# Performance work log

Measured on AMD Instinct MI355X. Metric: run time of the kernel, lower is better.

Reference implementation:

```python
import jax, jax.numpy as jnp
import numpy as np

N_NODES = 100000
N_EDGES = 1600000
IN_DIM = 128
HID = 64
N_GRAPHS = 64
OUT_DIM = 2


def setup_inputs() -> dict:
    key = jax.random.key(0)
    ks = jax.random.split(key, 16)
    x = jax.random.normal(ks[0], (N_NODES, IN_DIM), dtype=jnp.float32)
    edge_index = jax.random.randint(ks[1], (2, N_EDGES), 0, N_NODES, dtype=jnp.int64)
    batch = jnp.sort(jax.random.randint(ks[2], (N_NODES,), 0, N_GRAPHS, dtype=jnp.int64))
    def glorot(k, fan_in, fan_out):
        s = jnp.sqrt(6.0 / (fan_in + fan_out)).astype(jnp.float32)
        return jax.random.uniform(k, (fan_in, fan_out), jnp.float32, -s, s)
    return {
        "x": x, "edge_index": edge_index, "batch": batch,
        "W1": glorot(ks[3], IN_DIM, HID), "b1": jnp.zeros((HID,), jnp.float32),
        "W2": glorot(ks[4], HID, HID),   "b2": jnp.zeros((HID,), jnp.float32),
        "W3": glorot(ks[5], HID, HID),   "b3": jnp.zeros((HID,), jnp.float32),
        "Wc1": glorot(ks[6], HID, HID // 2), "bc1": jnp.zeros((HID // 2,), jnp.float32),
        "Wc2": glorot(ks[7], HID // 2, OUT_DIM), "bc2": jnp.zeros((OUT_DIM,), jnp.float32),
    }


def reference(x, edge_index, batch, W1, b1, W2, b2, W3, b3, Wc1, bc1, Wc2, bc2):
    n = x.shape[0]
    # GCNConv: add self-loops, symmetric deg^{-1/2} normalization
    loop = jnp.arange(n, dtype=edge_index.dtype)
    src = jnp.concatenate([edge_index[0], loop])  # [E+N]
    dst = jnp.concatenate([edge_index[1], loop])
    deg = jax.ops.segment_sum(jnp.ones_like(dst, dtype=x.dtype), dst, num_segments=n)
    dis = jnp.where(deg > 0, jax.lax.rsqrt(deg), 0.0)  # deg^{-1/2}
    norm = (dis[src] * dis[dst])[:, None]  # [E+N, 1]

    def conv(h, W, b):
        h = h @ W                                   # [N, F_out]
        msg = h[src] * norm                         # edge-wise gather
        return jax.ops.segment_sum(msg, dst, num_segments=n) + b  # scatter-add

    h = jax.nn.relu(conv(x, W1, b1))     # dropout is identity at inference
    h = jax.nn.relu(conv(h, W2, b2))
    h = conv(h, W3, b3)

    # global_mean_pool over batch ids
    sums = jax.ops.segment_sum(h, batch, num_segments=N_GRAPHS)
    cnts = jax.ops.segment_sum(jnp.ones((n,), h.dtype), batch, num_segments=N_GRAPHS)
    pooled = sums / jnp.maximum(cnts, 1.0)[:, None]  # [G, HID]

    # classifier MLP
    hcls = jax.nn.relu(pooled @ Wc1 + bc1)
    return hcls @ Wc2 + bc2  # [G, OUT_DIM]
```

## Files before the change

kernel.cpp:

```cpp
#include <hip/hip_runtime.h>
#include <hip/hip_bf16.h>

#define N_NODES 100000
#define N_EDGES 1600000
#define IN_DIM 128
#define HID 64
#define N_GRAPHS 64
#define OUT_DIM 2

#define NB_BUCKETS ((N_NODES + 255) / 256)
#define CHUNK 4096
#define NCHUNKS ((N_EDGES + CHUNK - 1) / CHUNK)
#define ARENA_CAP 6144


__device__ inline unsigned f2bf_rne(float f) {
    unsigned u = __float_as_uint(f);
    u += 0x7FFFu + ((u >> 16) & 1u);
    return u >> 16;
}
__device__ inline unsigned pack2(float lo, float hi) {
    return f2bf_rne(lo) | (f2bf_rne(hi) << 16);
}
__device__ inline float bf_lo(unsigned w) { return __uint_as_float(w << 16); }
__device__ inline float bf_hi(unsigned w) { return __uint_as_float(w & 0xFFFF0000u); }
__device__ inline float2 bf_pair(unsigned w) {
    return make_float2(bf_lo(w), bf_hi(w));
}
__device__ inline void acc2(float2& a, float2 b) { a.x += b.x; a.y += b.y; }


__global__ void kb_scan(const int* __restrict__ bcount, int* __restrict__ bbase) {
    int lane = threadIdx.x;
    int carry = 0;
    for (int c = 0; c < (NB_BUCKETS + 63) / 64; ++c) {
        int idx = c * 64 + lane;
        int v = (idx < NB_BUCKETS) ? bcount[idx] : 0;
        int orig = v;
        for (int d = 1; d < 64; d <<= 1) {
            int u = __shfl_up(v, d);
            if (lane >= d) v += u;
        }
        if (idx < NB_BUCKETS) bbase[idx] = v - orig + carry;
        carry += __shfl(v, 63);
    }
    if (lane == 0) bbase[NB_BUCKETS] = carry;
}

__global__ __launch_bounds__(256) void kb_scatter(const int* __restrict__ src,
                                                  const int* __restrict__ dst,
                                                  int* __restrict__ bcount,
                                                  unsigned* __restrict__ arena) {
    __shared__ unsigned staged[CHUNK];
    __shared__ unsigned short sbuck[CHUNK];
    __shared__ int hist[NB_BUCKETS];
    __shared__ int lofs[NB_BUCKETS];
    __shared__ int lcur[NB_BUCKETS];
    __shared__ int gbase[NB_BUCKETS];
    int t = threadIdx.x;
    int lane = t & 63, wv = t >> 6;
    for (int i = t; i < NB_BUCKETS; i += 256) hist[i] = 0;
    __syncthreads();
    int chunk0 = blockIdx.x * CHUNK;
    int cN = min(CHUNK, N_EDGES - chunk0);
    for (int i = t; i < cN; i += 256) atomicAdd(&hist[dst[chunk0 + i] >> 8], 1);
    __syncthreads();
    if (wv == 0) {
        int carry = 0;
        for (int c = 0; c < (NB_BUCKETS + 63) / 64; ++c) {
            int idx = c * 64 + lane;
            int v = (idx < NB_BUCKETS) ? hist[idx] : 0;
            int orig = v;
            for (int d = 1; d < 64; d <<= 1) {
                int u = __shfl_up(v, d);
                if (lane >= d) v += u;
            }
            if (idx < NB_BUCKETS) lofs[idx] = v - orig + carry;
            carry += __shfl(v, 63);
        }
    }
    __syncthreads();
    for (int i = t; i < NB_BUCKETS; i += 256) {
        lcur[i] = lofs[i];
        gbase[i] = hist[i] ? (atomicAdd(&bcount[i], hist[i]) + i * ARENA_CAP) : 0;
    }
    __syncthreads();
    for (int i = t; i < cN; i += 256) {
        int e = chunk0 + i;
        int d = dst[e];
        int b = d >> 8;
        int lp = atomicAdd(&lcur[b], 1);
        staged[lp] = ((unsigned)src[e] << 8) | (unsigned)(d & 255);
        sbuck[lp] = (unsigned short)b;
    }
    __syncthreads();
    for (int p = t; p < cN; p += 256) {
        int b = sbuck[p];
        arena[gbase[b] + (p - lofs[b])] = staged[p];
    }
}

__global__ __launch_bounds__(256) void k_bfin(const unsigned* __restrict__ arena,
                                              const int* __restrict__ bbase,
                                              int* __restrict__ ssrc,
                                              int* __restrict__ off,
                                              float* __restrict__ dis) {
    __shared__ int cnt[256];
    __shared__ int lofs[256];
    __shared__ int lcur[256];
    int t = threadIdx.x;
    int lane = t & 63, wv = t >> 6;
    cnt[t] = 0;
    __syncthreads();
    int b = blockIdx.x;
    int lo = bbase[b];
    int cntB = bbase[b + 1] - lo;
    const unsigned* ap = arena + (size_t)b * ARENA_CAP;
    for (int e = t; e < cntB; e += 256) atomicAdd(&cnt[ap[e] & 255], 1);
    __syncthreads();
    if (wv == 0) {
        int carry = 0;
#pragma unroll
        for (int c = 0; c < 4; ++c) {
            int idx = c * 64 + lane;
            int v = cnt[idx];
            int orig = v;
            for (int d = 1; d < 64; d <<= 1) {
                int u = __shfl_up(v, d);
                if (lane >= d) v += u;
            }
            lofs[idx] = v - orig + carry;
            carry += __shfl(v, 63);
        }
    }
    __syncthreads();
    lcur[t] = lofs[t];
    int node = b * 256 + t;
    if (node < N_NODES) {
        off[node] = lo + lofs[t];
        dis[node] = rsqrtf((float)cnt[t] + 1.0f);
    }
    if (b == NB_BUCKETS - 1 && t == 0) off[N_NODES] = N_EDGES;
    __syncthreads();
    for (int e = t; e < cntB; e += 256) {
        unsigned pk = ap[e];
        int p = atomicAdd(&lcur[pk & 255u], 1);
        ssrc[lo + p] = (int)(pk >> 8);
    }
}


__global__ __launch_bounds__(256) void k_wprep(const float* __restrict__ W1,
                                               const float* __restrict__ W2,
                                               const float* __restrict__ W3,
                                               unsigned short* __restrict__ Wt1,
                                               unsigned short* __restrict__ Wt2,
                                               unsigned short* __restrict__ Wt3) {
    int t = blockIdx.x * 256 + threadIdx.x;
    if (t < 64 * 128) {
        int n = t >> 7, k = t & 127;
        Wt1[t] = (unsigned short)f2bf_rne(W1[k * 64 + n]);
    }
    if (t < 64 * 64) {
        int n = t >> 6, k = t & 63;
        Wt2[t] = (unsigned short)f2bf_rne(W2[k * 64 + n]);
        Wt3[t] = (unsigned short)f2bf_rne(W3[k * 64 + n]);
    }
}

template <int K, bool AF32>
__global__ __launch_bounds__(256) void k_gemm(const void* __restrict__ Ain,
                                              const unsigned short* __restrict__ Wt,
                                              const float* __restrict__ dis,
                                              unsigned* __restrict__ g16) {
    constexpr int PITCH = K + 8;
    constexpr int ABYTES = 2 * 64 * PITCH * 2;
    constexpr int CBYTES = 64 * 68 * 4;
    constexpr int SMEM = ABYTES > CBYTES ? ABYTES : CBYTES;
    __shared__ __align__(16) char smem[SMEM];
    short* As = (short*)smem;
    short* Bs = As + 64 * PITCH;
    float* Cs = (float*)smem;
    constexpr int CP = 68;

    int t = threadIdx.x, lane = t & 63, w = t >> 6;
    int row0 = blockIdx.x * 64;

    constexpr int UN = 64 * (K / 8);
#pragma unroll
    for (int u = t; u < UN; u += 256) {
        int r = u / (K / 8), c = u % (K / 8);
        int grow = row0 + r;
        grow = grow < N_NODES ? grow : N_NODES - 1;
        uint4 o;
        if (AF32) {
            const float* Ap = (const float*)Ain + (size_t)grow * K + c * 8;
            float4 f0 = *(const float4*)Ap;
            float4 f1 = *(const float4*)(Ap + 4);
            o.x = pack2(f0.x, f0.y); o.y = pack2(f0.z, f0.w);
            o.z = pack2(f1.x, f1.y); o.w = pack2(f1.z, f1.w);
        } else {
            o = ((const uint4*)Ain)[(size_t)grow * (K / 8) + c];
        }
        *(uint4*)&As[r * PITCH + c * 8] = o;
    }
#pragma unroll
    for (int u = t; u < UN; u += 256) {
        int n = u / (K / 8), c = u % (K / 8);
        *(uint4*)&Bs[n * PITCH + c * 8] = *(const uint4*)&Wt[n * K + c * 8];
    }
    __syncthreads();

    using frag = __attribute__((ext_vector_type(8))) short;
    using fragc = __attribute__((ext_vector_type(4))) float;
    fragc z = {0.f, 0.f, 0.f, 0.f};
    fragc acc[4] = {z, z, z, z};
    int m = lane & 15, quad = lane >> 4;
#pragma unroll
    for (int ks = 0; ks < K / 32; ++ks) {
        frag a = *(frag*)&As[(w * 16 + m) * PITCH + ks * 32 + quad * 8];
#pragma unroll
        for (int nt = 0; nt < 4; ++nt) {
            frag b = *(frag*)&Bs[(nt * 16 + m) * PITCH + ks * 32 + quad * 8];
            acc[nt] = __builtin_amdgcn_mfma_f32_16x16x32_bf16(a, b, acc[nt], 0, 0, 0);
        }
    }
    __syncthreads();
#pragma unroll
    for (int nt = 0; nt < 4; ++nt)
#pragma unroll
        for (int reg = 0; reg < 4; ++reg)
            Cs[(w * 16 + quad * 4 + reg) * CP + nt * 16 + m] = acc[nt][reg];
    __syncthreads();

    {
        int r = t >> 2, c0 = (t & 3) * 16;
        int grow = row0 + r;
        if (grow < N_NODES) {
            float dr = dis[grow];
            const float* cp = &Cs[r * CP + c0];
            uint4 o0, o1;
            o0.x = pack2(cp[0] * dr, cp[1] * dr);
            o0.y = pack2(cp[2] * dr, cp[3] * dr);
            o0.z = pack2(cp[4] * dr, cp[5] * dr);
            o0.w = pack2(cp[6] * dr, cp[7] * dr);
            o1.x = pack2(cp[8] * dr, cp[9] * dr);
            o1.y = pack2(cp[10] * dr, cp[11] * dr);
            o1.z = pack2(cp[12] * dr, cp[13] * dr);
            o1.w = pack2(cp[14] * dr, cp[15] * dr);
            ((uint4*)g16)[(size_t)grow * 8 + (c0 >> 3)] = o0;
            ((uint4*)g16)[(size_t)grow * 8 + (c0 >> 3) + 1] = o1;
        }
    }
}

template <bool RELU>
__global__ __launch_bounds__(256) void k_aggr(const unsigned* __restrict__ g16,
                                              const int* __restrict__ off,
                                              const int* __restrict__ ssrc,
                                              const float* __restrict__ dis,
                                              const float* __restrict__ bias,
                                              unsigned* __restrict__ h16) {
    int lane = threadIdx.x & 63, wv = threadIdx.x >> 6;
    int r8 = lane >> 3;
    int li = lane & 7;
    int row = blockIdx.x * 32 + wv * 8 + r8;
    if (row >= N_NODES) return;
    const uint4* g4 = (const uint4*)g16;
    float2 acc[4] = {make_float2(0.f, 0.f), make_float2(0.f, 0.f),
                     make_float2(0.f, 0.f), make_float2(0.f, 0.f)};
    int lo = off[row], hi = off[row + 1];
    int e = lo;
    for (; e + 1 < hi; e += 2) {
        unsigned o0 = (unsigned)ssrc[e] * 8u + (unsigned)li;
        unsigned o1 = (unsigned)ssrc[e + 1] * 8u + (unsigned)li;
        uint4 v0 = g4[o0];
        uint4 v1 = g4[o1];
        acc2(acc[0], bf_pair(v0.x)); acc2(acc[0], bf_pair(v1.x));
        acc2(acc[1], bf_pair(v0.y)); acc2(acc[1], bf_pair(v1.y));
        acc2(acc[2], bf_pair(v0.z)); acc2(acc[2], bf_pair(v1.z));
        acc2(acc[3], bf_pair(v0.w)); acc2(acc[3], bf_pair(v1.w));
    }
    if (e < hi) {
        unsigned o = (unsigned)ssrc[e] * 8u + (unsigned)li;
        uint4 v = g4[o];
        acc2(acc[0], bf_pair(v.x));
        acc2(acc[1], bf_pair(v.y));
        acc2(acc[2], bf_pair(v.z));
        acc2(acc[3], bf_pair(v.w));
    }
    unsigned base = (unsigned)row * 8u + (unsigned)li;
    uint4 sv = g4[base];
    float2 sp[4] = {bf_pair(sv.x), bf_pair(sv.y), bf_pair(sv.z), bf_pair(sv.w)};
    float dr = dis[row];
    float4 b0 = ((const float4*)bias)[li * 2];
    float4 b1 = ((const float4*)bias)[li * 2 + 1];
    float bb[8] = {b0.x, b0.y, b0.z, b0.w, b1.x, b1.y, b1.z, b1.w};
    float o[8];
#pragma unroll
    for (int j = 0; j < 4; ++j) {
        o[2 * j]     = dr * (acc[j].x + sp[j].x) + bb[2 * j];
        o[2 * j + 1] = dr * (acc[j].y + sp[j].y) + bb[2 * j + 1];
    }
    if (RELU) {
#pragma unroll
        for (int j = 0; j < 8; ++j) o[j] = fmaxf(o[j], 0.f);
    }
    uint4 wvo;
    wvo.x = pack2(o[0], o[1]);
    wvo.y = pack2(o[2], o[3]);
    wvo.z = pack2(o[4], o[5]);
    wvo.w = pack2(o[6], o[7]);
    ((uint4*)h16)[base] = wvo;
}


__global__ __launch_bounds__(256) void k_pool1(const unsigned short* __restrict__ h16,
                                               const int* __restrict__ batch,
                                               float* __restrict__ sums) {
    int lane = threadIdx.x & 63, wv = threadIdx.x >> 6;
    int node0 = blockIdx.x * 256 + wv * 64;
    int node1 = min(node0 + 64, N_NODES);
    float acc = 0.f;
    int cur = -1;
    for (int i = node0; i < node1; ++i) {
        int bi = batch[i];
        if (bi != cur) {
            if (cur >= 0) atomicAdd(&sums[cur * HID + lane], acc);
            acc = 0.f;
            cur = bi;
        }
        unsigned u = h16[(size_t)i * HID + lane];
        acc += __uint_as_float(u << 16);
    }
    if (cur >= 0) atomicAdd(&sums[cur * HID + lane], acc);
}

__device__ inline int lower_bound_batch(const int* batch, int key) {
    int lo = 0, hi = N_NODES;
    while (lo < hi) {
        int mid = (lo + hi) >> 1;
        if (batch[mid] < key) lo = mid + 1;
        else hi = mid;
    }
    return lo;
}

__global__ __launch_bounds__(256) void k_cls(const float* __restrict__ sums,
                                             const int* __restrict__ batch,
                                             const float* __restrict__ Wc1,
                                             const float* __restrict__ bc1,
                                             const float* __restrict__ Wc2,
                                             const float* __restrict__ bc2,
                                             float* __restrict__ out) {
    __shared__ float pooled[N_GRAPHS][HID];
    __shared__ float hc[N_GRAPHS][HID / 2];
    __shared__ float cnts[N_GRAPHS];
    int t = threadIdx.x;
    if (t < N_GRAPHS) {
        int lo = lower_bound_batch(batch, t);
        int hi = lower_bound_batch(batch, t + 1);
        cnts[t] = fmaxf((float)(hi - lo), 1.0f);
    }
    __syncthreads();
    for (int idx = t; idx < N_GRAPHS * HID; idx += 256) {
        int gi = idx >> 6;
        pooled[gi][idx & 63] = sums[idx] / cnts[gi];
    }
    __syncthreads();
    for (int idx = t; idx < N_GRAPHS * (HID / 2); idx += 256) {
        int gi = idx >> 5, f = idx & 31;
        float a = bc1[f];
#pragma unroll
        for (int k = 0; k < HID; ++k) a = fmaf(pooled[gi][k], Wc1[k * (HID / 2) + f], a);
        hc[gi][f] = fmaxf(a, 0.f);
    }
    __syncthreads();
    for (int idx = t; idx < N_GRAPHS * OUT_DIM; idx += 256) {
        int gi = idx >> 1, f = idx & 1;
        float a = bc2[f];
#pragma unroll
        for (int k = 0; k < HID / 2; ++k) a = fmaf(hc[gi][k], Wc2[k * OUT_DIM + f], a);
        out[gi * OUT_DIM + f] = a;
    }
}


extern "C" void kernel_launch(void* const* d_in, const int* in_sizes, int n_in,
                              void* d_out, int out_size, void* d_ws, size_t ws_size,
                              hipStream_t stream) {
    const float* x    = (const float*)d_in[0];
    const int*   eidx = (const int*)d_in[1];
    const int*   batch= (const int*)d_in[2];
    const float* W1 = (const float*)d_in[3];  const float* b1 = (const float*)d_in[4];
    const float* W2 = (const float*)d_in[5];  const float* b2 = (const float*)d_in[6];
    const float* W3 = (const float*)d_in[7];  const float* b3 = (const float*)d_in[8];
    const float* Wc1 = (const float*)d_in[9];  const float* bc1 = (const float*)d_in[10];
    const float* Wc2 = (const float*)d_in[11]; const float* bc2 = (const float*)d_in[12];
    float* out = (float*)d_out;

    const int* esrc = eidx;
    const int* edst = eidx + N_EDGES;

    size_t o = 0;
    auto alloc = [&](size_t bytes) {
        void* p = (char*)d_ws + o;
        o += (bytes + 255) & ~(size_t)255;
        return p;
    };
    int*            bcount = (int*)alloc((size_t)NB_BUCKETS * 4);
    int*            bbase  = (int*)alloc((size_t)(NB_BUCKETS + 1) * 4);
    float*          dis    = (float*)alloc((size_t)N_NODES * 4);
    unsigned*       arena  = (unsigned*)alloc((size_t)NB_BUCKETS * ARENA_CAP * 4);
    int*            ssrc   = (int*)alloc((size_t)N_EDGES * 4);
    int*            off    = (int*)alloc((size_t)(N_NODES + 1) * 4);
    unsigned*       g16    = (unsigned*)alloc((size_t)N_NODES * HID * 2);
    unsigned*       h16    = (unsigned*)alloc((size_t)N_NODES * HID * 2);
    unsigned short* Wt1    = (unsigned short*)alloc((size_t)64 * 128 * 2);
    unsigned short* Wt2    = (unsigned short*)alloc((size_t)64 * 64 * 2);
    unsigned short* Wt3    = (unsigned short*)alloc((size_t)64 * 64 * 2);
    float*          sums   = (float*)alloc((size_t)N_GRAPHS * HID * 4);
    (void)ws_size;

    const int TB = 256;
    int gridG = (N_NODES + 63) / 64;
    int gridR = (N_NODES + 31) / 32;

    hipMemsetAsync(bcount, 0, (size_t)NB_BUCKETS * 4, stream);
    hipMemsetAsync(sums, 0, (size_t)N_GRAPHS * HID * 4, stream);
    k_wprep<<<32, TB, 0, stream>>>(W1, W2, W3, Wt1, Wt2, Wt3);
    kb_scatter<<<NCHUNKS, TB, 0, stream>>>(esrc, edst, bcount, arena);
    kb_scan<<<1, 64, 0, stream>>>(bcount, bbase);
    k_bfin<<<NB_BUCKETS, TB, 0, stream>>>(arena, bbase, ssrc, off, dis);

    k_gemm<IN_DIM, true><<<gridG, TB, 0, stream>>>(x, Wt1, dis, g16);
    k_aggr<true><<<gridR, TB, 0, stream>>>(g16, off, ssrc, dis, b1, h16);

    k_gemm<HID, false><<<gridG, TB, 0, stream>>>(h16, Wt2, dis, g16);
    k_aggr<true><<<gridR, TB, 0, stream>>>(g16, off, ssrc, dis, b2, h16);

    k_gemm<HID, false><<<gridG, TB, 0, stream>>>(h16, Wt3, dis, g16);
    k_aggr<false><<<gridR, TB, 0, stream>>>(g16, off, ssrc, dis, b3, h16);

    k_pool1<<<NB_BUCKETS, TB, 0, stream>>>((const unsigned short*)h16, batch, sums);
    k_cls<<<1, TB, 0, stream>>>(sums, batch, Wc1, bc1, Wc2, bc2, out);
}
```

Measured before the change: 333.2 us.

## Fuse aggregation with next layer's GEMM and unroll edge gather by four

Adds a k_aggr_gemm kernel that aggregates neighbour features for a 64-row tile, applies bias and ReLU, keeps the result in shared memory as bf16, and immediately multiplies by the next layer's weights with MFMA, writing the dis-scaled output. This removes two separate GEMM launches and the global write and re-read of the intermediate hidden activations. The edge gather loop is also unrolled from two to four loads to put more memory requests in flight. The trade-off is larger per-block shared memory and more registers, which may lower occupancy during the gather phase.

```diff
diff --git a/kernel.cpp b/kernel.cpp
--- a/kernel.cpp
+++ b/kernel.cpp
@@ -28,6 +28,10 @@
     return make_float2(bf_lo(w), bf_hi(w));
 }
 __device__ inline void acc2(float2& a, float2 b) { a.x += b.x; a.y += b.y; }
+__device__ inline void accv(float2 a[4], uint4 v) {
+    acc2(a[0], bf_pair(v.x)); acc2(a[1], bf_pair(v.y));
+    acc2(a[2], bf_pair(v.z)); acc2(a[3], bf_pair(v.w));
+}
 
 
 __global__ void kb_scan(const int* __restrict__ bcount, int* __restrict__ bbase) {
@@ -254,6 +258,119 @@
     }
 }
 
+__global__ __launch_bounds__(256) void k_aggr_gemm(const unsigned* __restrict__ gin,
+                                                   const int* __restrict__ off,
+                                                   const int* __restrict__ ssrc,
+                                                   const float* __restrict__ dis,
+                                                   const float* __restrict__ bias,
+                                                   const unsigned short* __restrict__ Wt,
+                                                   unsigned* __restrict__ gout) {
+    constexpr int K = HID;
+    constexpr int PITCH = K + 8;
+    constexpr int ABYTES = 2 * 64 * PITCH * 2;
+    constexpr int CBYTES = 64 * 68 * 4;
+    constexpr int SMEM = ABYTES > CBYTES ? ABYTES : CBYTES;
+    __shared__ __align__(16) char smem[SMEM];
+    short* As = (short*)smem;
+    short* Bs = As + 64 * PITCH;
+    float* Cs = (float*)smem;
+    constexpr int CP = 68;
+
+    int t = threadIdx.x, lane = t & 63, w = t >> 6;
+    int row0 = blockIdx.x * 64;
+    int r8 = lane >> 3, li = lane & 7;
+    const uint4* g4 = (const uint4*)gin;
+
+#pragma unroll
+    for (int u = t; u < 64 * 8; u += 256) {
+        int n = u >> 3, c = u & 7;
+        *(uint4*)&Bs[n * PITCH + c * 8] = *(const uint4*)&Wt[n * K + c * 8];
+    }
+
+    float4 b0 = ((const float4*)bias)[li * 2];
+    float4 b1 = ((const float4*)bias)[li * 2 + 1];
+#pragma unroll
+    for (int half = 0; half < 2; ++half) {
+        int r = w * 8 + r8 + half * 32;
+        int row = row0 + r;
+        int crow = row < N_NODES ? row : N_NODES - 1;
+        float2 acc[4] = {make_float2(0.f, 0.f), make_float2(0.f, 0.f),
+                         make_float2(0.f, 0.f), make_float2(0.f, 0.f)};
+        int lo = off[crow], hi = off[crow + 1];
+        int e = lo;
+        for (; e + 3 < hi; e += 4) {
+            unsigned o0 = (unsigned)ssrc[e] * 8u + (unsigned)li;
+            unsigned o1 = (unsigned)ssrc[e + 1] * 8u + (unsigned)li;
+            unsigned o2 = (unsigned)ssrc[e + 2] * 8u + (unsigned)li;
+            unsigned o3 = (unsigned)ssrc[e + 3] * 8u + (unsigned)li;
+            uint4 v0 = g4[o0], v1 = g4[o1], v2 = g4[o2], v3 = g4[o3];
+            accv(acc, v0); accv(acc, v1); accv(acc, v2); accv(acc, v3);
+        }
+        for (; e < hi; ++e) {
+            uint4 v = g4[(unsigned)ssrc[e] * 8u + (unsigned)li];
+            accv(acc, v);
+        }
+        uint4 sv = g4[(unsigned)crow * 8u + (unsigned)li];
+        float2 sp[4] = {bf_pair(sv.x), bf_pair(sv.y), bf_pair(sv.z), bf_pair(sv.w)};
+        float dr = dis[crow];
+        float bb[8] = {b0.x, b0.y, b0.z, b0.w, b1.x, b1.y, b1.z, b1.w};
+        float o[8];
+#pragma unroll
+        for (int j = 0; j < 4; ++j) {
+            o[2 * j]     = fmaxf(dr * (acc[j].x + sp[j].x) + bb[2 * j], 0.f);
+            o[2 * j + 1] = fmaxf(dr * (acc[j].y + sp[j].y) + bb[2 * j + 1], 0.f);
+        }
+        uint4 hv;
+        hv.x = pack2(o[0], o[1]);
+        hv.y = pack2(o[2], o[3]);
+        hv.z = pack2(o[4], o[5]);
+        hv.w = pack2(o[6], o[7]);
+        *(uint4*)&As[r * PITCH + li * 8] = hv;
+    }
+    __syncthreads();
+
+    using frag = __attribute__((ext_vector_type(8))) short;
+    using fragc = __attribute__((ext_vector_type(4))) float;
+    fragc z = {0.f, 0.f, 0.f, 0.f};
+    fragc acc[4] = {z, z, z, z};
+    int m = lane & 15, quad = lane >> 4;
+#pragma unroll
+    for (int ks = 0; ks < K / 32; ++ks) {
+        frag a = *(frag*)&As[(w * 16 + m) * PITCH + ks * 32 + quad * 8];
+#pragma unroll
+        for (int nt = 0; nt < 4; ++nt) {
+            frag b = *(frag*)&Bs[(nt * 16 + m) * PITCH + ks * 32 + quad * 8];
+            acc[nt] = __builtin_amdgcn_mfma_f32_16x16x32_bf16(a, b, acc[nt], 0, 0, 0);
+        }
+    }
+    __syncthreads();
+#pragma unroll
+    for (int nt = 0; nt < 4; ++nt)
+#pragma unroll
+        for (int reg = 0; reg < 4; ++reg)
+            Cs[(w * 16 + quad * 4 + reg) * CP + nt * 16 + m] = acc[nt][reg];
+    __syncthreads();
+    {
+        int r = t >> 2, c0 = (t & 3) * 16;
+        int grow = row0 + r;
+        if (grow < N_NODES) {
+            float dr = dis[grow];
+            const float* cp = &Cs[r * CP + c0];
+            uint4 o0, o1;
+            o0.x = pack2(cp[0] * dr, cp[1] * dr);
+            o0.y = pack2(cp[2] * dr, cp[3] * dr);
+            o0.z = pack2(cp[4] * dr, cp[5] * dr);
+            o0.w = pack2(cp[6] * dr, cp[7] * dr);
+            o1.x = pack2(cp[8] * dr, cp[9] * dr);
+            o1.y = pack2(cp[10] * dr, cp[11] * dr);
+            o1.z = pack2(cp[12] * dr, cp[13] * dr);
+            o1.w = pack2(cp[14] * dr, cp[15] * dr);
+            ((uint4*)gout)[(size_t)grow * 8 + (c0 >> 3)] = o0;
+            ((uint4*)gout)[(size_t)grow * 8 + (c0 >> 3) + 1] = o1;
+        }
+    }
+}
+
 template <bool RELU>
 __global__ __launch_bounds__(256) void k_aggr(const unsigned* __restrict__ g16,
                                               const int* __restrict__ off,
@@ -271,23 +388,17 @@
                      make_float2(0.f, 0.f), make_float2(0.f, 0.f)};
     int lo = off[row], hi = off[row + 1];
     int e = lo;
-    for (; e + 1 < hi; e += 2) {
+    for (; e + 3 < hi; e += 4) {
         unsigned o0 = (unsigned)ssrc[e] * 8u + (unsigned)li;
         unsigned o1 = (unsigned)ssrc[e + 1] * 8u + (unsigned)li;
-        uint4 v0 = g4[o0];
-        uint4 v1 = g4[o1];
-        acc2(acc[0], bf_pair(v0.x)); acc2(acc[0], bf_pair(v1.x));
-        acc2(acc[1], bf_pair(v0.y)); acc2(acc[1], bf_pair(v1.y));
-        acc2(acc[2], bf_pair(v0.z)); acc2(acc[2], bf_pair(v1.z));
-        acc2(acc[3], bf_pair(v0.w)); acc2(acc[3], bf_pair(v1.w));
-    }
-    if (e < hi) {
-        unsigned o = (unsigned)ssrc[e] * 8u + (unsigned)li;
-        uint4 v = g4[o];
-        acc2(acc[0], bf_pair(v.x));
-        acc2(acc[1], bf_pair(v.y));
-        acc2(acc[2], bf_pair(v.z));
-        acc2(acc[3], bf_pair(v.w));
+        unsigned o2 = (unsigned)ssrc[e + 2] * 8u + (unsigned)li;
+        unsigned o3 = (unsigned)ssrc[e + 3] * 8u + (unsigned)li;
+        uint4 v0 = g4[o0], v1 = g4[o1], v2 = g4[o2], v3 = g4[o3];
+        accv(acc, v0); accv(acc, v1); accv(acc, v2); accv(acc, v3);
+    }
+    for (; e < hi; ++e) {
+        uint4 v = g4[(unsigned)ssrc[e] * 8u + (unsigned)li];
+        accv(acc, v);
     }
     unsigned base = (unsigned)row * 8u + (unsigned)li;
     uint4 sv = g4[base];
@@ -414,8 +525,8 @@
     unsigned*       arena  = (unsigned*)alloc((size_t)NB_BUCKETS * ARENA_CAP * 4);
     int*            ssrc   = (int*)alloc((size_t)N_EDGES * 4);
     int*            off    = (int*)alloc((size_t)(N_NODES + 1) * 4);
-    unsigned*       g16    = (unsigned*)alloc((size_t)N_NODES * HID * 2);
-    unsigned*       h16    = (unsigned*)alloc((size_t)N_NODES * HID * 2);
+    unsigned*       gA     = (unsigned*)alloc((size_t)N_NODES * HID * 2);
+    unsigned*       gB     = (unsigned*)alloc((size_t)N_NODES * HID * 2);
     unsigned short* Wt1    = (unsigned short*)alloc((size_t)64 * 128 * 2);
     unsigned short* Wt2    = (unsigned short*)alloc((size_t)64 * 64 * 2);
     unsigned short* Wt3    = (unsigned short*)alloc((size_t)64 * 64 * 2);
@@ -433,15 +544,14 @@
     kb_scan<<<1, 64, 0, stream>>>(bcount, bbase);
     k_bfin<<<NB_BUCKETS, TB, 0, stream>>>(arena, bbase, ssrc, off, dis);
 
-    k_gemm<IN_DIM, true><<<gridG, TB, 0, stream>>>(x, Wt1, dis, g16);
-    k_aggr<true><<<gridR, TB, 0, stream>>>(g16, off, ssrc, dis, b1, h16);
-
-    k_gemm<HID, false><<<gridG, TB, 0, stream>>>(h16, Wt2, dis, g16);
-    k_aggr<true><<<gridR, TB, 0, stream>>>(g16, off, ssrc, dis, b2, h16);
-
-    k_gemm<HID, false><<<gridG, TB, 0, stream>>>(h16, Wt3, dis, g16);
-    k_aggr<false><<<gridR, TB, 0, stream>>>(g16, off, ssrc, dis, b3, h16);
-
-    k_pool1<<<NB_BUCKETS, TB, 0, stream>>>((const unsigned short*)h16, batch, sums);
+    k_gemm<IN_DIM, true><<<gridG, TB, 0, stream>>>(x, Wt1, dis, gA);
+
+    k_aggr_gemm<<<gridG, TB, 0, stream>>>(gA, off, ssrc, dis, b1, Wt2, gB);
+
+    k_aggr_gemm<<<gridG, TB, 0, stream>>>(gB, off, ssrc, dis, b2, Wt3, gA);
+
+    k_aggr<false><<<gridR, TB, 0, stream>>>(gA, off, ssrc, dis, b3, gB);
+
+    k_pool1<<<NB_BUCKETS, TB, 0, stream>>>((const unsigned short*)gB, batch, sums);
     k_cls<<<1, TB, 0, stream>>>(sums, batch, Wc1, bc1, Wc2, bc2, out);
 }
```

Measured after the change: 320.7 us. -3.7%, faster.
